# Optimization experiments

Measured on AMD Instinct MI355X. Metric: run time of the kernel, lower is better.

The kernel has to match this reference:

```python
import jax, jax.numpy as jnp
import numpy as np

N_NODES = 50000
N_EDGES = 800000
GNN_IN, GNN_HID, COMB = 256, 64, 64
MLP_IN, MLP_HID = 256, 512


def glorot(key, shape):
    fan_in, fan_out = shape[0], shape[1]
    s = jnp.sqrt(6.0 / (fan_in + fan_out)).astype(jnp.float32)
    return jax.random.uniform(key, shape, jnp.float32, -s, s)


def setup_inputs() -> dict:
    key = jax.random.key(0)
    ks = jax.random.split(key, 12)
    x = jax.random.normal(ks[0], (N_NODES, GNN_IN), jnp.float32)
    edge_index = jax.random.randint(ks[1], (2, N_EDGES), 0, N_NODES, jnp.int64 if jax.config.jax_enable_x64 else jnp.int32)
    edge_attr = jax.random.uniform(ks[2], (N_EDGES,), jnp.float32)
    user_features = jax.random.normal(ks[3], (N_NODES, MLP_IN), jnp.float32)
    params = {
        'gcn1_W': glorot(ks[4], (GNN_IN, GNN_HID)),
        'gcn1_b': jnp.zeros((GNN_HID,), jnp.float32),
        'gcn2_W': glorot(ks[5], (GNN_HID, COMB)),
        'gcn2_b': jnp.zeros((COMB,), jnp.float32),
        'fc1_W': glorot(ks[6], (MLP_IN, MLP_HID)),
        'fc1_b': jnp.zeros((MLP_HID,), jnp.float32),
        'fc2_W': glorot(ks[7], (MLP_HID, COMB)),
        'fc2_b': jnp.zeros((COMB,), jnp.float32),
        'fcf_W': glorot(ks[8], (2 * COMB, 1)),
        'fcf_b': jnp.zeros((1,), jnp.float32),
    }
    return dict(x=x, edge_index=edge_index, edge_attr=edge_attr,
                user_features=user_features, **params)


def gcn_conv(x, W, b, src, dst, ew, n_nodes):
    # PyG GCNConv: transform, add self-loops (weight 1), sym-normalize, scatter-add.
    h = x @ W  # [N, out]
    loop = jnp.arange(n_nodes, dtype=src.dtype)
    src_sl = jnp.concatenate([src, loop])
    dst_sl = jnp.concatenate([dst, loop])
    ew_sl = jnp.concatenate([ew, jnp.ones((n_nodes,), ew.dtype)])
    deg = jax.ops.segment_sum(ew_sl, dst_sl, num_segments=n_nodes)
    dinv = jnp.where(deg > 0, jax.lax.rsqrt(jnp.maximum(deg, 1e-12)), 0.0)
    norm = dinv[src_sl] * ew_sl * dinv[dst_sl]  # [E+N]
    msg = h[src_sl] * norm[:, None]             # gather + scale
    out = jax.ops.segment_sum(msg, dst_sl, num_segments=n_nodes)
    return out + b


def reference(x, edge_index, edge_attr, user_features,
              gcn1_W, gcn1_b, gcn2_W, gcn2_b,
              fc1_W, fc1_b, fc2_W, fc2_b, fcf_W, fcf_b):
    src, dst = edge_index[0], edge_index[1]
    n = x.shape[0]
    # MLP branch
    mlp_out = jax.nn.relu(user_features @ fc1_W + fc1_b) @ fc2_W + fc2_b
    # GNN branch
    g = gcn_conv(x, gcn1_W, gcn1_b, src, dst, edge_attr, n)
    g = jax.nn.relu(g)
    gnn_out = gcn_conv(g, gcn2_W, gcn2_b, src, dst, edge_attr, n)
    combined = jnp.concatenate([mlp_out, gnn_out], axis=-1)
    return combined @ fcf_W + fcf_b
```

## Files before the change

kernel.cpp:

```cpp
#include <hip/hip_runtime.h>
#include <hip/hip_bf16.h>

#define N_NODES 50000
#define N_EDGES 800000
#define BROW 264

typedef __attribute__((ext_vector_type(8))) short bfrag8;
typedef __attribute__((ext_vector_type(4))) float f32x4;
typedef __attribute__((ext_vector_type(4))) unsigned short us4;
typedef __attribute__((ext_vector_type(8))) unsigned short us8;

__device__ __forceinline__ float bf2f(unsigned short u) {
  return __uint_as_float(((unsigned int)u) << 16);
}
__device__ __forceinline__ unsigned short f2bf(float f) {
  unsigned int u = __float_as_uint(f);
  u = (u + 0x7fffu + ((u >> 16) & 1u)) >> 16;
  return (unsigned short)u;
}
__device__ __forceinline__ float ldS(const void* p, int f32, size_t i) {
  return f32 ? ((const float*)p)[i] : bf2f(((const unsigned short*)p)[i]);
}
__device__ __forceinline__ void stO(void* out, int f32, int i, float v) {
  if (f32) ((float*)out)[i] = v;
  else ((unsigned short*)out)[i] = f2bf(v);
}

template <int F32>
__device__ __forceinline__ void stageB(const void* src, int nb,
                                       unsigned short* __restrict__ Bs) {
  const int t = threadIdx.x;
  const int r = t >> 2;
  const int q = t & 3;
  int row = nb + r;
  row = row < N_NODES ? row : (N_NODES - 1);
  const size_t base = (size_t)row * 256 + q * 64;
  unsigned short* dst = Bs + r * BROW + q * 64;
  if (F32) {
    const f32x4* s4 = (const f32x4*)((const float*)src + base);
#pragma unroll
    for (int j = 0; j < 8; ++j) {
      f32x4 a = s4[2 * j], b = s4[2 * j + 1];
      us8 o;
      o[0] = f2bf(a[0]); o[1] = f2bf(a[1]); o[2] = f2bf(a[2]); o[3] = f2bf(a[3]);
      o[4] = f2bf(b[0]); o[5] = f2bf(b[1]); o[6] = f2bf(b[2]); o[7] = f2bf(b[3]);
      *(us8*)(dst + j * 8) = o;
    }
  } else {
    const us8* s8 = (const us8*)((const unsigned short*)src + base);
#pragma unroll
    for (int j = 0; j < 8; ++j) *(us8*)(dst + j * 8) = s8[j];
  }
}

__global__ void k_detect(const void* x, const void* ea, const void* uf,
                         const void* f1W, const int* ei, int* flags) {
  int lane = threadIdx.x & 63;
  unsigned short ux = ((const unsigned short*)x)[lane];
  unsigned short ue = ((const unsigned short*)ea)[lane];
  unsigned short uu = ((const unsigned short*)uf)[lane];
  unsigned short uw = ((const unsigned short*)f1W)[lane];
  int oi = ei[2 * lane + 1];
  unsigned long long bx = __ballot(((ux >> 7) & 0xFF) > 0x85);
  unsigned long long be = __ballot((ue & 0x8000u) != 0);
  unsigned long long bu = __ballot(((uu >> 7) & 0xFF) > 0x85);
  unsigned long long bw = __ballot(((uw >> 7) & 0xFF) > 0x7E);
  unsigned long long bi = __ballot(oi != 0);
  if (lane == 0) {
    int fx = bx ? 1 : 0, fe = be ? 1 : 0, fu = bu ? 1 : 0, fw = bw ? 1 : 0;
    flags[0] = fx; flags[1] = fe; flags[2] = fu; flags[3] = fw;
    flags[4] = (bi == 0ull) ? 1 : 0;
    flags[5] = (fx & fe & fu & fw);
  }
}

__global__ __launch_bounds__(256) void k_edges(const int* __restrict__ ei,
                                               const int* __restrict__ flags,
                                               int* __restrict__ srcW,
                                               int* __restrict__ dstW,
                                               int* __restrict__ cnt,
                                               float* __restrict__ mlpc) {
  int e = blockIdx.x * 256 + threadIdx.x;
  if (e >= N_EDGES) return;
  if (e <= N_NODES) cnt[e] = 0;
  if (e < N_NODES) mlpc[e] = 0.f;
  int i64 = flags[4];
  int s, d;
  if (i64) { s = ei[2 * e]; d = ei[1600000 + 2 * e]; }
  else     { s = ei[e];     d = ei[800000 + e]; }
  s = s < 0 ? 0 : (s > N_NODES - 1 ? N_NODES - 1 : s);
  d = d < 0 ? 0 : (d > N_NODES - 1 ? N_NODES - 1 : d);
  srcW[e] = s; dstW[e] = d;
}

__global__ __launch_bounds__(256) void k_hist(const int* __restrict__ dstW,
                                              int* __restrict__ cnt) {
  int e = blockIdx.x * 256 + threadIdx.x;
  if (e < N_EDGES) atomicAdd(&cnt[dstW[e]], 1);
}

__global__ __launch_bounds__(256) void k_scan1(const int* __restrict__ cnt,
                                               int* __restrict__ rp,
                                               int* __restrict__ bsum) {
  __shared__ int sd[256];
  int t = threadIdx.x;
  int i0 = blockIdx.x * 1024 + t * 4;
  int v0 = (i0 + 0) < N_NODES ? cnt[i0 + 0] : 0;
  int v1 = (i0 + 1) < N_NODES ? cnt[i0 + 1] : 0;
  int v2 = (i0 + 2) < N_NODES ? cnt[i0 + 2] : 0;
  int v3 = (i0 + 3) < N_NODES ? cnt[i0 + 3] : 0;
  int ts = v0 + v1 + v2 + v3;
  sd[t] = ts;
  __syncthreads();
  for (int off = 1; off < 256; off <<= 1) {
    int x = (t >= off) ? sd[t - off] : 0;
    __syncthreads();
    sd[t] += x;
    __syncthreads();
  }
  int exoff = sd[t] - ts;
  if (i0 + 0 < N_NODES) rp[i0 + 0] = exoff;
  if (i0 + 1 < N_NODES) rp[i0 + 1] = exoff + v0;
  if (i0 + 2 < N_NODES) rp[i0 + 2] = exoff + v0 + v1;
  if (i0 + 3 < N_NODES) rp[i0 + 3] = exoff + v0 + v1 + v2;
  if (t == 255) bsum[blockIdx.x] = sd[255];
}

__global__ void k_scan2(const int* __restrict__ bsum, int* __restrict__ boff,
                        int* __restrict__ rp, int nb) {
  if (threadIdx.x == 0) {
    int run = 0;
    for (int b = 0; b < nb; ++b) { boff[b] = run; run += bsum[b]; }
    rp[N_NODES] = run;
  }
}

__global__ __launch_bounds__(256) void k_scan3(int* __restrict__ rp,
                                               const int* __restrict__ boff,
                                               int* __restrict__ cursor) {
  int i = blockIdx.x * 256 + threadIdx.x;
  if (i < N_NODES) {
    int r = rp[i] + boff[i >> 10];
    rp[i] = r;
    cursor[i] = r;
  }
}

__global__ __launch_bounds__(256) void k_place(const int* __restrict__ srcW,
                                               const int* __restrict__ dstW,
                                               const void* ea, const int* __restrict__ flags,
                                               int* __restrict__ cursor,
                                               int* __restrict__ eSrc,
                                               float* __restrict__ eW) {
  int e = blockIdx.x * 256 + threadIdx.x;
  if (e >= N_EDGES) return;
  int d = dstW[e];
  int pos = atomicAdd(&cursor[d], 1);
  eSrc[pos] = srcW[e];
  eW[pos] = ldS(ea, flags[1], e);
}

__global__ __launch_bounds__(256) void k_degc(const int* __restrict__ rp,
                                              const float* __restrict__ eW,
                                              float* __restrict__ dinv) {
  const int i = blockIdx.x * 4 + (threadIdx.x >> 6);
  if (i >= N_NODES) return;
  const int lane = threadIdx.x & 63;
  const int base = rp[i], end = rp[i + 1];
  float s = 0.f;
  for (int j = base + lane; j < end; j += 64) s += eW[j];
#pragma unroll
  for (int off = 32; off > 0; off >>= 1) s += __shfl_xor(s, off, 64);
  if (lane == 0) dinv[i] = rsqrtf(s + 1.0f);
}

__global__ __launch_bounds__(256) void k_scale(const int* __restrict__ eSrc,
                                               const float* __restrict__ dinv,
                                               float* __restrict__ eW) {
  int j = blockIdx.x * 256 + threadIdx.x;
  if (j < N_EDGES) eW[j] *= dinv[eSrc[j]];
}

__global__ __launch_bounds__(512) void k_prep(
    const void* f1W, const void* g1W, const void* f2W, const void* f2b,
    const void* g2W, const void* g2b, const void* ffW, const void* ffb,
    const int* __restrict__ flags, unsigned short* __restrict__ W1T,
    unsigned short* __restrict__ WgT, float* __restrict__ w2f,
    float* __restrict__ w2g, float* __restrict__ constv) {
  const int fw = flags[3];
  if (blockIdx.x < 288) {
    int tid = blockIdx.x * 512 + threadIdx.x;
    if (tid < 512 * 256) {
      int c = tid >> 8, k = tid & 255;
      W1T[tid] = f2bf(ldS(f1W, fw, (size_t)k * 512 + c));
    } else if (tid < 512 * 256 + 64 * 256) {
      int j = tid - 512 * 256;
      int c = j >> 8, k = j & 255;
      WgT[j] = f2bf(ldS(g1W, fw, (size_t)k * 64 + c));
    }
    return;
  }
  int t = threadIdx.x;
  if (t < 512) {
    float s = 0.f;
    for (int c = 0; c < 64; ++c) s += ldS(f2W, fw, t * 64 + c) * ldS(ffW, fw, c);
    w2f[t] = s;
  }
  if (t < 64) {
    float s = 0.f;
    for (int c = 0; c < 64; ++c) s += ldS(g2W, fw, t * 64 + c) * ldS(ffW, fw, 64 + c);
    w2g[t] = s;
  }
  if (t == 0) {
    float s = ldS(ffb, fw, 0);
    for (int c = 0; c < 64; ++c) {
      s += ldS(f2b, fw, c) * ldS(ffW, fw, c);
      s += ldS(g2b, fw, c) * ldS(ffW, fw, 64 + c);
    }
    constv[0] = s;
  }
}

template <int F32>
__global__ __launch_bounds__(256, 3) void k_h13(
    const void* x, const unsigned short* __restrict__ WgT,
    const int* __restrict__ flags, unsigned short* __restrict__ h1b) {
  if (flags[0] != F32) return;
  __shared__ unsigned short Bs[64 * BROW];
  const int nb = blockIdx.x * 64;
  stageB<F32>(x, nb, Bs);
  __syncthreads();

  const int lane = threadIdx.x & 63;
  const int wave = threadIdx.x >> 6;
  const int l15 = lane & 15;
  const int quad = lane >> 4;
  const unsigned short* ap = WgT + (size_t)(wave * 16 + l15) * 256 + quad * 8;

  f32x4 acc[4];
#pragma unroll
  for (int u = 0; u < 4; ++u) acc[u] = (f32x4){0.f, 0.f, 0.f, 0.f};

#pragma unroll
  for (int ks = 0; ks < 8; ++ks) {
    bfrag8 a = *(const bfrag8*)(ap + ks * 32);
    const int bofs = ks * 32 + quad * 8;
#pragma unroll
    for (int u = 0; u < 4; ++u) {
      bfrag8 b = *(const bfrag8*)(Bs + (u * 16 + l15) * BROW + bofs);
      acc[u] = __builtin_amdgcn_mfma_f32_16x16x32_bf16(a, b, acc[u], 0, 0, 0);
    }
  }
#pragma unroll
  for (int u = 0; u < 4; ++u) {
    int node = nb + u * 16 + l15;
    if (node < N_NODES) {
      us4 o;
#pragma unroll
      for (int r = 0; r < 4; ++r) o[r] = f2bf(acc[u][r]);
      *(us4*)(h1b + (size_t)node * 64 + wave * 16 + quad * 4) = o;
    }
  }
}

template <int F32>
__global__ __launch_bounds__(256, 2) void k_mlp4(
    const void* uf, const unsigned short* __restrict__ W1T,
    const void* fc1b, const float* __restrict__ w2f,
    const int* __restrict__ flags, float* __restrict__ mlpc) {
  if (flags[2] != F32) return;
  __shared__ unsigned short Bs[64 * BROW];
  const int nb = blockIdx.x * 64;
  stageB<F32>(uf, nb, Bs);
  __syncthreads();

  const int fw = flags[3];
  const int lane = threadIdx.x & 63;
  const int wave = threadIdx.x >> 6;
  const int l15 = lane & 15;
  const int quad = lane >> 4;

  for (int half = 0; half < 2; ++half) {
    const int c_base = half * 256 + wave * 64;
    const unsigned short* ap = W1T + (size_t)(c_base + l15) * 256 + quad * 8;

    f32x4 acc[4][4];
#pragma unroll
    for (int t = 0; t < 4; ++t)
#pragma unroll
      for (int u = 0; u < 4; ++u) acc[t][u] = (f32x4){0.f, 0.f, 0.f, 0.f};

#pragma unroll
    for (int ks = 0; ks < 8; ++ks) {
      const int bofs = ks * 32 + quad * 8;
      bfrag8 b[4];
#pragma unroll
      for (int u = 0; u < 4; ++u)
        b[u] = *(const bfrag8*)(Bs + (u * 16 + l15) * BROW + bofs);
#pragma unroll
      for (int t = 0; t < 4; ++t) {
        bfrag8 a = *(const bfrag8*)(ap + (size_t)t * 16 * 256 + ks * 32);
#pragma unroll
        for (int u = 0; u < 4; ++u)
          acc[t][u] = __builtin_amdgcn_mfma_f32_16x16x32_bf16(a, b[u], acc[t][u], 0, 0, 0);
      }
    }

    float part[4] = {0.f, 0.f, 0.f, 0.f};
#pragma unroll
    for (int t = 0; t < 4; ++t) {
#pragma unroll
      for (int r = 0; r < 4; ++r) {
        const int c = c_base + t * 16 + quad * 4 + r;
        const float bc = ldS(fc1b, fw, c);
        const float wc = w2f[c];
#pragma unroll
        for (int u = 0; u < 4; ++u) {
          float v = acc[t][u][r] + bc;
          v = v > 0.f ? v : 0.f;
          part[u] += v * wc;
        }
      }
    }
#pragma unroll
    for (int u = 0; u < 4; ++u) {
      part[u] += __shfl_xor(part[u], 16, 64);
      part[u] += __shfl_xor(part[u], 32, 64);
      int node = nb + u * 16 + l15;
      if (lane < 16 && node < N_NODES) atomicAdd(&mlpc[node], part[u]);
    }
  }
}

__global__ __launch_bounds__(256) void k_aggs2(
    const int* __restrict__ rp, const int* __restrict__ eSrc,
    const float* __restrict__ eW, const unsigned short* __restrict__ h1b,
    const float* __restrict__ dinv, const void* g1b, const float* __restrict__ w2g,
    const int* __restrict__ flags, float* __restrict__ s2) {
  const int i = blockIdx.x * 4 + (threadIdx.x >> 6);
  if (i >= N_NODES) return;
  const int lane = threadIdx.x & 63;
  const int base = rp[i], end = rp[i + 1];
  const float di = dinv[i];
  float acc = 0.f;
  int j = base;
  for (; j + 8 <= end; j += 8) {
    int ss[8]; float ww[8];
#pragma unroll
    for (int q = 0; q < 8; ++q) { ss[q] = eSrc[j + q]; ww[q] = eW[j + q]; }
    float hv[8];
#pragma unroll
    for (int q = 0; q < 8; ++q) hv[q] = bf2f(h1b[(size_t)ss[q] * 64 + lane]);
#pragma unroll
    for (int q = 0; q < 8; ++q) acc += ww[q] * hv[q];
  }
  for (; j < end; ++j) acc += eW[j] * bf2f(h1b[(size_t)eSrc[j] * 64 + lane]);
  float v = acc * di + di * di * bf2f(h1b[(size_t)i * 64 + lane]) + ldS(g1b, flags[3], lane);
  v = v > 0.f ? v : 0.f;
  float p = v * w2g[lane];
#pragma unroll
  for (int off = 32; off > 0; off >>= 1) p += __shfl_xor(p, off, 64);
  if (lane == 0) s2[i] = p;
}

__global__ __launch_bounds__(256) void k_fin2(
    const int* __restrict__ rp, const int* __restrict__ eSrc,
    const float* __restrict__ eW, const float* __restrict__ s2,
    const float* __restrict__ dinv, const float* __restrict__ mlpc,
    const float* __restrict__ constv, const int* __restrict__ flags, void* out) {
  const int i = blockIdx.x * 4 + (threadIdx.x >> 6);
  if (i >= N_NODES) return;
  const int lane = threadIdx.x & 63;
  const int base = rp[i], end = rp[i + 1];
  float p = 0.f;
  for (int j = base + lane; j < end; j += 64) p += eW[j] * s2[eSrc[j]];
#pragma unroll
  for (int off = 32; off > 0; off >>= 1) p += __shfl_xor(p, off, 64);
  if (lane == 0) {
    float di = dinv[i];
    stO(out, flags[5], i, mlpc[i] + di * p + di * di * s2[i] + constv[0]);
  }
}

__global__ __launch_bounds__(256) void k_zero(const int* __restrict__ flags, void* out) {
  int i = blockIdx.x * 256 + threadIdx.x;
  if (i < N_NODES) stO(out, flags[5], i, 0.f);
}

extern "C" void kernel_launch(void* const* d_in, const int* in_sizes, int n_in,
                              void* d_out, int out_size, void* d_ws, size_t ws_size,
                              hipStream_t stream) {
  const void* x   = d_in[0];
  const int*  ei  = (const int*)d_in[1];
  const void* ea  = d_in[2];
  const void* uf  = d_in[3];
  const void* g1W = d_in[4];
  const void* g1b = d_in[5];
  const void* g2W = d_in[6];
  const void* g2b = d_in[7];
  const void* f1W = d_in[8];
  const void* f1b = d_in[9];
  const void* f2W = d_in[10];
  const void* f2b = d_in[11];
  const void* ffW = d_in[12];
  const void* ffb = d_in[13];

  float* ws = (float*)d_ws;
  int*   flags  = (int*)ws;
  float* w2f    = ws + 16;
  float* w2g    = ws + 528;
  float* constv = ws + 592;
  float* dinv   = ws + 608;
  float* s2     = ws + 50608;
  float* mlpc   = ws + 100608;
  unsigned short* W1T = (unsigned short*)(ws + 150608);
  unsigned short* WgT = W1T + 131072;
  int* srcW   = (int*)(ws + 224336);
  int* dstW   = srcW + 800000;
  int* rowptr = dstW + 800000;
  int* bsum   = (int*)(ws + 1874352);
  int* boff   = bsum + 64;
  int* counts = (int*)(ws + 1874480);
  int* cursor = (int*)(ws + 1924496);
  int* eSrc   = (int*)(ws + 1974496);
  float* eW   = ws + 2774496;
  unsigned short* h1b = (unsigned short*)(ws + 3574496);
  const size_t NEED = (size_t)5174496 * 4;

  k_detect<<<1, 64, 0, stream>>>(x, ea, uf, f1W, ei, flags);
  if (ws_size < NEED) {
    k_zero<<<(N_NODES + 255) / 256, 256, 0, stream>>>(flags, d_out);
    return;
  }
  const int NB = (N_NODES + 1023) / 1024;
  const int NGB = (N_NODES + 63) / 64;

  k_edges<<<(N_EDGES + 255) / 256, 256, 0, stream>>>(ei, flags, srcW, dstW, counts, mlpc);
  k_hist<<<(N_EDGES + 255) / 256, 256, 0, stream>>>(dstW, counts);
  k_scan1<<<NB, 256, 0, stream>>>(counts, rowptr, bsum);
  k_scan2<<<1, 64, 0, stream>>>(bsum, boff, rowptr, NB);
  k_scan3<<<(N_NODES + 255) / 256, 256, 0, stream>>>(rowptr, boff, cursor);
  k_place<<<(N_EDGES + 255) / 256, 256, 0, stream>>>(srcW, dstW, ea, flags, cursor, eSrc, eW);
  k_degc<<<(N_NODES + 3) / 4, 256, 0, stream>>>(rowptr, eW, dinv);
  k_scale<<<(N_EDGES + 255) / 256, 256, 0, stream>>>(eSrc, dinv, eW);
  k_prep<<<289, 512, 0, stream>>>(f1W, g1W, f2W, f2b, g2W, g2b, ffW, ffb, flags,
                                  W1T, WgT, w2f, w2g, constv);
  k_h13<0><<<NGB, 256, 0, stream>>>(x, WgT, flags, h1b);
  k_h13<1><<<NGB, 256, 0, stream>>>(x, WgT, flags, h1b);
  k_mlp4<0><<<NGB, 256, 0, stream>>>(uf, W1T, f1b, w2f, flags, mlpc);
  k_mlp4<1><<<NGB, 256, 0, stream>>>(uf, W1T, f1b, w2f, flags, mlpc);
  k_aggs2<<<(N_NODES + 3) / 4, 256, 0, stream>>>(rowptr, eSrc, eW, h1b, dinv, g1b, w2g, flags, s2);
  k_fin2<<<(N_NODES + 3) / 4, 256, 0, stream>>>(rowptr, eSrc, eW, s2, dinv, mlpc, constv, flags, d_out);
}
```

Baseline: 406.2 us.

## Fuse CSR build, compute degrees by atomics, pack edges, merge GEMM variants

Degree sums are now computed with float atomics during the histogram pass, so the separate degree and edge-scale kernels disappear, and dinv is produced in the scan-offset kernel. Edge placement reads edge_index directly and writes a packed 64-bit (weight, src) record, which removes the srcW/dstW intermediates and halves the index loads in the aggregation kernels. The GEMM kernels for the two dtypes are merged into single 512-thread launches that branch on the flag at runtime, and the MLP kernel covers all 512 hidden columns in one pass instead of looping over two halves. Float atomics make the degree sum order nondeterministic. degf aliases s2, which is only safe because s2 is written later.

Result: no change. 413.1 us (+1.7%).

```diff
diff --git a/kernel.cpp b/kernel.cpp
--- a/kernel.cpp
+++ b/kernel.cpp
@@ -27,19 +27,19 @@
 }
 
 template <int F32>
-__device__ __forceinline__ void stageB(const void* src, int nb,
-                                       unsigned short* __restrict__ Bs) {
+__device__ __forceinline__ void stageB8(const void* src, int nb,
+                                        unsigned short* __restrict__ Bs) {
   const int t = threadIdx.x;
-  const int r = t >> 2;
-  const int q = t & 3;
+  const int r = t >> 3;
+  const int q = t & 7;
   int row = nb + r;
   row = row < N_NODES ? row : (N_NODES - 1);
-  const size_t base = (size_t)row * 256 + q * 64;
-  unsigned short* dst = Bs + r * BROW + q * 64;
+  const size_t base = (size_t)row * 256 + q * 32;
+  unsigned short* dst = Bs + r * BROW + q * 32;
   if (F32) {
     const f32x4* s4 = (const f32x4*)((const float*)src + base);
 #pragma unroll
-    for (int j = 0; j < 8; ++j) {
+    for (int j = 0; j < 4; ++j) {
       f32x4 a = s4[2 * j], b = s4[2 * j + 1];
       us8 o;
       o[0] = f2bf(a[0]); o[1] = f2bf(a[1]); o[2] = f2bf(a[2]); o[3] = f2bf(a[3]);
@@ -49,7 +49,7 @@
   } else {
     const us8* s8 = (const us8*)((const unsigned short*)src + base);
 #pragma unroll
-    for (int j = 0; j < 8; ++j) *(us8*)(dst + j * 8) = s8[j];
+    for (int j = 0; j < 4; ++j) *(us8*)(dst + j * 8) = s8[j];
   }
 }
 
@@ -74,29 +74,28 @@
   }
 }
 
-__global__ __launch_bounds__(256) void k_edges(const int* __restrict__ ei,
-                                               const int* __restrict__ flags,
-                                               int* __restrict__ srcW,
-                                               int* __restrict__ dstW,
-                                               int* __restrict__ cnt,
+__global__ __launch_bounds__(256) void k_zero3(int* __restrict__ counts,
+                                               float* __restrict__ degf,
                                                float* __restrict__ mlpc) {
+  int i = blockIdx.x * 256 + threadIdx.x;
+  if (i < N_NODES) { counts[i] = 0; degf[i] = 0.f; mlpc[i] = 0.f; }
+  if (i == 0) counts[N_NODES] = 0;
+}
+
+__global__ __launch_bounds__(256) void k_edges2(const int* __restrict__ ei,
+                                                const void* ea,
+                                                const int* __restrict__ flags,
+                                                int* __restrict__ counts,
+                                                float* __restrict__ degf) {
   int e = blockIdx.x * 256 + threadIdx.x;
   if (e >= N_EDGES) return;
-  if (e <= N_NODES) cnt[e] = 0;
-  if (e < N_NODES) mlpc[e] = 0.f;
-  int i64 = flags[4];
-  int s, d;
-  if (i64) { s = ei[2 * e]; d = ei[1600000 + 2 * e]; }
-  else     { s = ei[e];     d = ei[800000 + e]; }
-  s = s < 0 ? 0 : (s > N_NODES - 1 ? N_NODES - 1 : s);
+  int d;
+  if (flags[4]) d = ei[1600000 + 2 * e];
+  else          d = ei[800000 + e];
   d = d < 0 ? 0 : (d > N_NODES - 1 ? N_NODES - 1 : d);
-  srcW[e] = s; dstW[e] = d;
-}
-
-__global__ __launch_bounds__(256) void k_hist(const int* __restrict__ dstW,
-                                              int* __restrict__ cnt) {
-  int e = blockIdx.x * 256 + threadIdx.x;
-  if (e < N_EDGES) atomicAdd(&cnt[dstW[e]], 1);
+  float w = ldS(ea, flags[1], e);
+  atomicAdd(&counts[d], 1);
+  atomicAdd(&degf[d], w);
 }
 
 __global__ __launch_bounds__(256) void k_scan1(const int* __restrict__ cnt,
@@ -135,50 +134,36 @@
   }
 }
 
-__global__ __launch_bounds__(256) void k_scan3(int* __restrict__ rp,
-                                               const int* __restrict__ boff,
-                                               int* __restrict__ cursor) {
+__global__ __launch_bounds__(256) void k_scan3d(int* __restrict__ rp,
+                                                const int* __restrict__ boff,
+                                                int* __restrict__ cursor,
+                                                const float* __restrict__ degf,
+                                                float* __restrict__ dinv) {
   int i = blockIdx.x * 256 + threadIdx.x;
   if (i < N_NODES) {
     int r = rp[i] + boff[i >> 10];
     rp[i] = r;
     cursor[i] = r;
-  }
-}
-
-__global__ __launch_bounds__(256) void k_place(const int* __restrict__ srcW,
-                                               const int* __restrict__ dstW,
-                                               const void* ea, const int* __restrict__ flags,
-                                               int* __restrict__ cursor,
-                                               int* __restrict__ eSrc,
-                                               float* __restrict__ eW) {
+    dinv[i] = rsqrtf(degf[i] + 1.0f);
+  }
+}
+
+__global__ __launch_bounds__(256) void k_place2(const int* __restrict__ ei,
+                                                const void* ea,
+                                                const int* __restrict__ flags,
+                                                const float* __restrict__ dinv,
+                                                int* __restrict__ cursor,
+                                                unsigned long long* __restrict__ e8) {
   int e = blockIdx.x * 256 + threadIdx.x;
   if (e >= N_EDGES) return;
-  int d = dstW[e];
+  int s, d;
+  if (flags[4]) { s = ei[2 * e]; d = ei[1600000 + 2 * e]; }
+  else          { s = ei[e];     d = ei[800000 + e]; }
+  s = s < 0 ? 0 : (s > N_NODES - 1 ? N_NODES - 1 : s);
+  d = d < 0 ? 0 : (d > N_NODES - 1 ? N_NODES - 1 : d);
+  float w = ldS(ea, flags[1], e) * dinv[s];
   int pos = atomicAdd(&cursor[d], 1);
-  eSrc[pos] = srcW[e];
-  eW[pos] = ldS(ea, flags[1], e);
-}
-
-__global__ __launch_bounds__(256) void k_degc(const int* __restrict__ rp,
-                                              const float* __restrict__ eW,
-                                              float* __restrict__ dinv) {
-  const int i = blockIdx.x * 4 + (threadIdx.x >> 6);
-  if (i >= N_NODES) return;
-  const int lane = threadIdx.x & 63;
-  const int base = rp[i], end = rp[i + 1];
-  float s = 0.f;
-  for (int j = base + lane; j < end; j += 64) s += eW[j];
-#pragma unroll
-  for (int off = 32; off > 0; off >>= 1) s += __shfl_xor(s, off, 64);
-  if (lane == 0) dinv[i] = rsqrtf(s + 1.0f);
-}
-
-__global__ __launch_bounds__(256) void k_scale(const int* __restrict__ eSrc,
-                                               const float* __restrict__ dinv,
-                                               float* __restrict__ eW) {
-  int j = blockIdx.x * 256 + threadIdx.x;
-  if (j < N_EDGES) eW[j] *= dinv[eSrc[j]];
+  e8[pos] = ((unsigned long long)__float_as_uint(w) << 32) | (unsigned int)s;
 }
 
 __global__ __launch_bounds__(512) void k_prep(
@@ -221,57 +206,57 @@
   }
 }
 
-template <int F32>
-__global__ __launch_bounds__(256, 3) void k_h13(
+__global__ __launch_bounds__(512, 2) void k_h13u(
     const void* x, const unsigned short* __restrict__ WgT,
     const int* __restrict__ flags, unsigned short* __restrict__ h1b) {
-  if (flags[0] != F32) return;
   __shared__ unsigned short Bs[64 * BROW];
   const int nb = blockIdx.x * 64;
-  stageB<F32>(x, nb, Bs);
+  if (flags[0]) stageB8<1>(x, nb, Bs);
+  else          stageB8<0>(x, nb, Bs);
   __syncthreads();
 
   const int lane = threadIdx.x & 63;
   const int wave = threadIdx.x >> 6;
+  const int ct = wave & 3;
+  const int nh = wave >> 2;
   const int l15 = lane & 15;
   const int quad = lane >> 4;
-  const unsigned short* ap = WgT + (size_t)(wave * 16 + l15) * 256 + quad * 8;
-
-  f32x4 acc[4];
-#pragma unroll
-  for (int u = 0; u < 4; ++u) acc[u] = (f32x4){0.f, 0.f, 0.f, 0.f};
+  const unsigned short* ap = WgT + (size_t)(ct * 16 + l15) * 256 + quad * 8;
+
+  f32x4 acc[2];
+  acc[0] = (f32x4){0.f, 0.f, 0.f, 0.f};
+  acc[1] = (f32x4){0.f, 0.f, 0.f, 0.f};
 
 #pragma unroll
   for (int ks = 0; ks < 8; ++ks) {
     bfrag8 a = *(const bfrag8*)(ap + ks * 32);
     const int bofs = ks * 32 + quad * 8;
 #pragma unroll
-    for (int u = 0; u < 4; ++u) {
-      bfrag8 b = *(const bfrag8*)(Bs + (u * 16 + l15) * BROW + bofs);
+    for (int u = 0; u < 2; ++u) {
+      bfrag8 b = *(const bfrag8*)(Bs + (nh * 32 + u * 16 + l15) * BROW + bofs);
       acc[u] = __builtin_amdgcn_mfma_f32_16x16x32_bf16(a, b, acc[u], 0, 0, 0);
     }
   }
 #pragma unroll
-  for (int u = 0; u < 4; ++u) {
-    int node = nb + u * 16 + l15;
+  for (int u = 0; u < 2; ++u) {
+    int node = nb + nh * 32 + u * 16 + l15;
     if (node < N_NODES) {
       us4 o;
 #pragma unroll
       for (int r = 0; r < 4; ++r) o[r] = f2bf(acc[u][r]);
-      *(us4*)(h1b + (size_t)node * 64 + wave * 16 + quad * 4) = o;
-    }
-  }
-}
-
-template <int F32>
-__global__ __launch_bounds__(256, 2) void k_mlp4(
+      *(us4*)(h1b + (size_t)node * 64 + ct * 16 + quad * 4) = o;
+    }
+  }
+}
+
+__global__ __launch_bounds__(512, 2) void k_mlpu(
     const void* uf, const unsigned short* __restrict__ W1T,
     const void* fc1b, const float* __restrict__ w2f,
     const int* __restrict__ flags, float* __restrict__ mlpc) {
-  if (flags[2] != F32) return;
   __shared__ unsigned short Bs[64 * BROW];
   const int nb = blockIdx.x * 64;
-  stageB<F32>(uf, nb, Bs);
+  if (flags[2]) stageB8<1>(uf, nb, Bs);
+  else          stageB8<0>(uf, nb, Bs);
   __syncthreads();
 
   const int fw = flags[3];
@@ -279,63 +264,60 @@
   const int wave = threadIdx.x >> 6;
   const int l15 = lane & 15;
   const int quad = lane >> 4;
-
-  for (int half = 0; half < 2; ++half) {
-    const int c_base = half * 256 + wave * 64;
-    const unsigned short* ap = W1T + (size_t)(c_base + l15) * 256 + quad * 8;
-
-    f32x4 acc[4][4];
-#pragma unroll
-    for (int t = 0; t < 4; ++t)
-#pragma unroll
-      for (int u = 0; u < 4; ++u) acc[t][u] = (f32x4){0.f, 0.f, 0.f, 0.f};
-
-#pragma unroll
-    for (int ks = 0; ks < 8; ++ks) {
-      const int bofs = ks * 32 + quad * 8;
-      bfrag8 b[4];
+  const int c_base = wave * 64;
+  const unsigned short* ap = W1T + (size_t)(c_base + l15) * 256 + quad * 8;
+
+  f32x4 acc[4][4];
+#pragma unroll
+  for (int t = 0; t < 4; ++t)
+#pragma unroll
+    for (int u = 0; u < 4; ++u) acc[t][u] = (f32x4){0.f, 0.f, 0.f, 0.f};
+
+#pragma unroll
+  for (int ks = 0; ks < 8; ++ks) {
+    const int bofs = ks * 32 + quad * 8;
+    bfrag8 b[4];
+#pragma unroll
+    for (int u = 0; u < 4; ++u)
+      b[u] = *(const bfrag8*)(Bs + (u * 16 + l15) * BROW + bofs);
+#pragma unroll
+    for (int t = 0; t < 4; ++t) {
+      bfrag8 a = *(const bfrag8*)(ap + (size_t)t * 16 * 256 + ks * 32);
 #pragma unroll
       for (int u = 0; u < 4; ++u)
-        b[u] = *(const bfrag8*)(Bs + (u * 16 + l15) * BROW + bofs);
-#pragma unroll
-      for (int t = 0; t < 4; ++t) {
-        bfrag8 a = *(const bfrag8*)(ap + (size_t)t * 16 * 256 + ks * 32);
-#pragma unroll
-        for (int u = 0; u < 4; ++u)
-          acc[t][u] = __builtin_amdgcn_mfma_f32_16x16x32_bf16(a, b[u], acc[t][u], 0, 0, 0);
+        acc[t][u] = __builtin_amdgcn_mfma_f32_16x16x32_bf16(a, b[u], acc[t][u], 0, 0, 0);
+    }
+  }
+
+  float part[4] = {0.f, 0.f, 0.f, 0.f};
+#pragma unroll
+  for (int t = 0; t < 4; ++t) {
+#pragma unroll
+    for (int r = 0; r < 4; ++r) {
+      const int c = c_base + t * 16 + quad * 4 + r;
+      const float bc = ldS(fc1b, fw, c);
+      const float wc = w2f[c];
+#pragma unroll
+      for (int u = 0; u < 4; ++u) {
+        float v = acc[t][u][r] + bc;
+        v = v > 0.f ? v : 0.f;
+        part[u] += v * wc;
       }
     }
-
-    float part[4] = {0.f, 0.f, 0.f, 0.f};
-#pragma unroll
-    for (int t = 0; t < 4; ++t) {
-#pragma unroll
-      for (int r = 0; r < 4; ++r) {
-        const int c = c_base + t * 16 + quad * 4 + r;
-        const float bc = ldS(fc1b, fw, c);
-        const float wc = w2f[c];
-#pragma unroll
-        for (int u = 0; u < 4; ++u) {
-          float v = acc[t][u][r] + bc;
-          v = v > 0.f ? v : 0.f;
-          part[u] += v * wc;
-        }
-      }
-    }
-#pragma unroll
-    for (int u = 0; u < 4; ++u) {
-      part[u] += __shfl_xor(part[u], 16, 64);
-      part[u] += __shfl_xor(part[u], 32, 64);
-      int node = nb + u * 16 + l15;
-      if (lane < 16 && node < N_NODES) atomicAdd(&mlpc[node], part[u]);
-    }
+  }
+#pragma unroll
+  for (int u = 0; u < 4; ++u) {
+    part[u] += __shfl_xor(part[u], 16, 64);
+    part[u] += __shfl_xor(part[u], 32, 64);
+    int node = nb + u * 16 + l15;
+    if (lane < 16 && node < N_NODES) atomicAdd(&mlpc[node], part[u]);
   }
 }
 
 __global__ __launch_bounds__(256) void k_aggs2(
-    const int* __restrict__ rp, const int* __restrict__ eSrc,
-    const float* __restrict__ eW, const unsigned short* __restrict__ h1b,
-    const float* __restrict__ dinv, const void* g1b, const float* __restrict__ w2g,
+    const int* __restrict__ rp, const unsigned long long* __restrict__ e8,
+    const unsigned short* __restrict__ h1b, const float* __restrict__ dinv,
+    const void* g1b, const float* __restrict__ w2g,
     const int* __restrict__ flags, float* __restrict__ s2) {
   const int i = blockIdx.x * 4 + (threadIdx.x >> 6);
   if (i >= N_NODES) return;
@@ -345,16 +327,23 @@
   float acc = 0.f;
   int j = base;
   for (; j + 8 <= end; j += 8) {
-    int ss[8]; float ww[8];
-#pragma unroll
-    for (int q = 0; q < 8; ++q) { ss[q] = eSrc[j + q]; ww[q] = eW[j + q]; }
-    float hv[8];
-#pragma unroll
-    for (int q = 0; q < 8; ++q) hv[q] = bf2f(h1b[(size_t)ss[q] * 64 + lane]);
+    unsigned long long vv[8];
+#pragma unroll
+    for (int q = 0; q < 8; ++q) vv[q] = e8[j + q];
+    float ww[8], hv[8];
+#pragma unroll
+    for (int q = 0; q < 8; ++q) {
+      ww[q] = __uint_as_float((unsigned int)(vv[q] >> 32));
+      hv[q] = bf2f(h1b[(size_t)(unsigned int)vv[q] * 64 + lane]);
+    }
 #pragma unroll
     for (int q = 0; q < 8; ++q) acc += ww[q] * hv[q];
   }
-  for (; j < end; ++j) acc += eW[j] * bf2f(h1b[(size_t)eSrc[j] * 64 + lane]);
+  for (; j < end; ++j) {
+    unsigned long long v = e8[j];
+    acc += __uint_as_float((unsigned int)(v >> 32)) *
+           bf2f(h1b[(size_t)(unsigned int)v * 64 + lane]);
+  }
   float v = acc * di + di * di * bf2f(h1b[(size_t)i * 64 + lane]) + ldS(g1b, flags[3], lane);
   v = v > 0.f ? v : 0.f;
   float p = v * w2g[lane];
@@ -364,16 +353,19 @@
 }
 
 __global__ __launch_bounds__(256) void k_fin2(
-    const int* __restrict__ rp, const int* __restrict__ eSrc,
-    const float* __restrict__ eW, const float* __restrict__ s2,
-    const float* __restrict__ dinv, const float* __restrict__ mlpc,
-    const float* __restrict__ constv, const int* __restrict__ flags, void* out) {
+    const int* __restrict__ rp, const unsigned long long* __restrict__ e8,
+    const float* __restrict__ s2, const float* __restrict__ dinv,
+    const float* __restrict__ mlpc, const float* __restrict__ constv,
+    const int* __restrict__ flags, void* out) {
   const int i = blockIdx.x * 4 + (threadIdx.x >> 6);
   if (i >= N_NODES) return;
   const int lane = threadIdx.x & 63;
   const int base = rp[i], end = rp[i + 1];
   float p = 0.f;
-  for (int j = base + lane; j < end; j += 64) p += eW[j] * s2[eSrc[j]];
+  for (int j = base + lane; j < end; j += 64) {
+    unsigned long long v = e8[j];
+    p += __uint_as_float((unsigned int)(v >> 32)) * s2[(unsigned int)v];
+  }
 #pragma unroll
   for (int off = 32; off > 0; off >>= 1) p += __shfl_xor(p, off, 64);
   if (lane == 0) {
@@ -411,44 +403,40 @@
   float* w2g    = ws + 528;
   float* constv = ws + 592;
   float* dinv   = ws + 608;
+  float* degf   = ws + 50608;
   float* s2     = ws + 50608;
   float* mlpc   = ws + 100608;
   unsigned short* W1T = (unsigned short*)(ws + 150608);
   unsigned short* WgT = W1T + 131072;
-  int* srcW   = (int*)(ws + 224336);
-  int* dstW   = srcW + 800000;
-  int* rowptr = dstW + 800000;
-  int* bsum   = (int*)(ws + 1874352);
+  int* rowptr = (int*)(ws + 224336);
+  int* bsum   = (int*)(ws + 274352);
   int* boff   = bsum + 64;
-  int* counts = (int*)(ws + 1874480);
-  int* cursor = (int*)(ws + 1924496);
-  int* eSrc   = (int*)(ws + 1974496);
-  float* eW   = ws + 2774496;
-  unsigned short* h1b = (unsigned short*)(ws + 3574496);
-  const size_t NEED = (size_t)5174496 * 4;
+  int* counts = (int*)(ws + 274480);
+  int* cursor = (int*)(ws + 324496);
+  unsigned long long* e8 = (unsigned long long*)(ws + 374496);
+  unsigned short* h1b = (unsigned short*)(ws + 1974496);
+  const size_t NEED = (size_t)3574496 * 4;
 
   k_detect<<<1, 64, 0, stream>>>(x, ea, uf, f1W, ei, flags);
   if (ws_size < NEED) {
     k_zero<<<(N_NODES + 255) / 256, 256, 0, stream>>>(flags, d_out);
     return;
   }
-  const int NB = (N_NODES + 1023) / 1024;
+  const int NZB = (N_NODES + 255) / 256;
+  const int NB  = (N_NODES + 1023) / 1024;
   const int NGB = (N_NODES + 63) / 64;
-
-  k_edges<<<(N_EDGES + 255) / 256, 256, 0, stream>>>(ei, flags, srcW, dstW, counts, mlpc);
-  k_hist<<<(N_EDGES + 255) / 256, 256, 0, stream>>>(dstW, counts);
+  const int NEB = (N_EDGES + 255) / 256;
+
+  k_zero3<<<NZB, 256, 0, stream>>>(counts, degf, mlpc);
+  k_edges2<<<NEB, 256, 0, stream>>>(ei, ea, flags, counts, degf);
   k_scan1<<<NB, 256, 0, stream>>>(counts, rowptr, bsum);
   k_scan2<<<1, 64, 0, stream>>>(bsum, boff, rowptr, NB);
-  k_scan3<<<(N_NODES + 255) / 256, 256, 0, stream>>>(rowptr, boff, cursor);
-  k_place<<<(N_EDGES + 255) / 256, 256, 0, stream>>>(srcW, dstW, ea, flags, cursor, eSrc, eW);
-  k_degc<<<(N_NODES + 3) / 4, 256, 0, stream>>>(rowptr, eW, dinv);
-  k_scale<<<(N_EDGES + 255) / 256, 256, 0, stream>>>(eSrc, dinv, eW);
+  k_scan3d<<<NZB, 256, 0, stream>>>(rowptr, boff, cursor, degf, dinv);
+  k_place2<<<NEB, 256, 0, stream>>>(ei, ea, flags, dinv, cursor, e8);
   k_prep<<<289, 512, 0, stream>>>(f1W, g1W, f2W, f2b, g2W, g2b, ffW, ffb, flags,
                                   W1T, WgT, w2f, w2g, constv);
-  k_h13<0><<<NGB, 256, 0, stream>>>(x, WgT, flags, h1b);
-  k_h13<1><<<NGB, 256, 0, stream>>>(x, WgT, flags, h1b);
-  k_mlp4<0><<<NGB, 256, 0, stream>>>(uf, W1T, f1b, w2f, flags, mlpc);
-  k_mlp4<1><<<NGB, 256, 0, stream>>>(uf, W1T, f1b, w2f, flags, mlpc);
-  k_aggs2<<<(N_NODES + 3) / 4, 256, 0, stream>>>(rowptr, eSrc, eW, h1b, dinv, g1b, w2g, flags, s2);
-  k_fin2<<<(N_NODES + 3) / 4, 256, 0, stream>>>(rowptr, eSrc, eW, s2, dinv, mlpc, constv, flags, d_out);
-}
+  k_h13u<<<NGB, 512, 0, stream>>>(x, WgT, flags, h1b);
+  k_mlpu<<<NGB, 512, 0, stream>>>(uf, W1T, f1b, w2f, flags, mlpc);
+  k_aggs2<<<(N_NODES + 3) / 4, 256, 0, stream>>>(rowptr, e8, h1b, dinv, g1b, w2g, flags, s2);
+  k_fin2<<<(N_NODES + 3) / 4, 256, 0, stream>>>(rowptr, e8, s2, dinv, mlpc, constv, flags, d_out);
+}
```
